# Kernel optimization log

Measured on AMD Instinct MI355X. Metric: run time of the kernel, lower is better.

## Reference

```python
import jax, jax.numpy as jnp
import numpy as np

INPUT_DIM, HIDDEN, OUT_DIM = 7, 64, 4


def _lstm_layer(x_seq, W_ih, W_hh, b_ih, b_hh):
    """Single LSTM layer, batch_first x_seq [B,T,D] -> [B,T,H]. PyTorch gate order i,f,g,o."""
    B = x_seq.shape[0]
    H = W_hh.shape[1]
    # Precompute input projection for all timesteps (hoist GEMM out of the scan).
    x_proj = jnp.einsum('btd,gd->btg', x_seq, W_ih) + b_ih + b_hh  # [B,T,4H]

    def step(carry, xt):
        h, c = carry
        gates = xt + h @ W_hh.T  # [B,4H]
        i, f, g, o = jnp.split(gates, 4, axis=-1)
        i = jax.nn.sigmoid(i)
        f = jax.nn.sigmoid(f)
        g = jnp.tanh(g)
        o = jax.nn.sigmoid(o)
        c = f * c + i * g
        h = o * jnp.tanh(c)
        return (h, c), h

    h0 = jnp.zeros((B, H), x_seq.dtype)
    c0 = jnp.zeros((B, H), x_seq.dtype)
    (_, _), hs = jax.lax.scan(step, (h0, c0), jnp.swapaxes(x_proj, 0, 1))  # hs [T,B,H]
    return jnp.swapaxes(hs, 0, 1)  # [B,T,H]


def setup_inputs() -> dict:
    key = jax.random.key(0)
    ks = jax.random.split(key, 12)
    s = 0.1  # init scale ~ 1/sqrt(hidden)
    x = jax.random.normal(ks[0], (4096, 512, INPUT_DIM), dtype=jnp.float32)
    W_ih0 = jax.random.normal(ks[1], (4 * HIDDEN, INPUT_DIM), dtype=jnp.float32) * s
    W_hh0 = jax.random.normal(ks[2], (4 * HIDDEN, HIDDEN), dtype=jnp.float32) * s
    b_ih0 = jax.random.normal(ks[3], (4 * HIDDEN,), dtype=jnp.float32) * s
    b_hh0 = jax.random.normal(ks[4], (4 * HIDDEN,), dtype=jnp.float32) * s
    W_ih1 = jax.random.normal(ks[5], (4 * HIDDEN, HIDDEN), dtype=jnp.float32) * s
    W_hh1 = jax.random.normal(ks[6], (4 * HIDDEN, HIDDEN), dtype=jnp.float32) * s
    b_ih1 = jax.random.normal(ks[7], (4 * HIDDEN,), dtype=jnp.float32) * s
    b_hh1 = jax.random.normal(ks[8], (4 * HIDDEN,), dtype=jnp.float32) * s
    W_fc = jax.random.normal(ks[9], (OUT_DIM, HIDDEN), dtype=jnp.float32) * s
    b_fc = jax.random.normal(ks[10], (OUT_DIM,), dtype=jnp.float32) * s
    return {"x": x, "W_ih0": W_ih0, "W_hh0": W_hh0, "b_ih0": b_ih0, "b_hh0": b_hh0,
            "W_ih1": W_ih1, "W_hh1": W_hh1, "b_ih1": b_ih1, "b_hh1": b_hh1,
            "W_fc": W_fc, "b_fc": b_fc}


def reference(x, W_ih0, W_hh0, b_ih0, b_hh0, W_ih1, W_hh1, b_ih1, b_hh1, W_fc, b_fc):
    h1 = _lstm_layer(x, W_ih0, W_hh0, b_ih0, b_hh0)   # [B,T,H]
    h2 = _lstm_layer(h1, W_ih1, W_hh1, b_ih1, b_hh1)  # [B,T,H]
    last = h2[:, -1, :]                               # [B,H]
    return last @ W_fc.T + b_fc                       # [B,4]
```

## Files before the change

### kernel.cpp

```cpp
#include <hip/hip_runtime.h>

#define T_SEQ 512
#define HID 64
#define MB 16
#define NTHREADS 1024
#define A1STR 104
#define A2STR 72

typedef __attribute__((ext_vector_type(8))) short short8;
typedef __attribute__((ext_vector_type(4))) float floatx4;

#define LOG2E 1.4426950408889634f

__device__ __forceinline__ short f2bf_rne(float v) {
  unsigned u = __float_as_uint(v);
  return (short)((u + 0x7FFFu + ((u >> 16) & 1u)) >> 16);
}
__device__ __forceinline__ float rcp_(float x) { return __builtin_amdgcn_rcpf(x); }
__device__ __forceinline__ float sigm_p(float ap) {
  return rcp_(1.f + __builtin_amdgcn_exp2f(-ap));
}
__device__ __forceinline__ float tanh_p(float yp) {
  return 1.f - 2.f * rcp_(__builtin_amdgcn_exp2f(yp) + 1.f);
}
__device__ __forceinline__ float tanh_c(float c) {
  return tanh_p((2.f * LOG2E) * c);
}

__device__ __forceinline__ int uofp(int p) {
  return (p & ~7) + ((p & 7) >> 1) + ((p & 1) << 2);
}

__device__ __forceinline__ short w1elem(int k, int n, float wsc,
                                        const float* __restrict__ Wih0,
                                        const float* __restrict__ Whh0) {
  float v;
  if      (k < 64) { v = Whh0[n*64 + uofp(k)]; }
  else if (k < 71) { v = Wih0[n*7 + (k - 64)]; }
  else return (short)0;
  return f2bf_rne(v * wsc);
}
__device__ __forceinline__ short w2elem(int k, int n, float wsc,
                                        const float* __restrict__ Wih1,
                                        const float* __restrict__ Whh1) {
  float v;
  if (k < 64) { v = Wih1[n*64 + uofp(k)]; }
  else        { v = Whh1[n*64 + uofp(k - 64)]; }
  return f2bf_rne(v * wsc);
}

#define MFMA(A, B, C) __builtin_amdgcn_mfma_f32_16x16x32_bf16((A), (B), (C), 0, 0, 0)

#define PACK2(ha, hb)                                                        \
  ((unsigned)(unsigned short)f2bf_rne(ha) |                                  \
   ((unsigned)(unsigned short)f2bf_rne(hb) << 16))

__global__ __launch_bounds__(NTHREADS, 4) void lstm_fused(
    const float* __restrict__ x,
    const float* __restrict__ Wih0, const float* __restrict__ Whh0,
    const float* __restrict__ bih0, const float* __restrict__ bhh0,
    const float* __restrict__ Wih1, const float* __restrict__ Whh1,
    const float* __restrict__ bih1, const float* __restrict__ bhh1,
    const float* __restrict__ Wfc,  const float* __restrict__ bfc,
    float* __restrict__ out)
{
  __shared__ __align__(16) short A1[2][MB][A1STR];
  __shared__ __align__(16) short A2[2][MB][A2STR];
  __shared__ float h2f[MB][HID + 4];

  const int tid  = threadIdx.x;
  const int lane = tid & 63;
  const int wave = tid >> 6;
  const int wl   = wave & 7;
  const bool isL1 = wave < 8;
  const int l15  = lane & 15;
  const int quad = lane >> 4;
  const int quad8= quad * 8;
  const int g4   = l15 & 3;
  const int b0   = blockIdx.x * MB;
  const int u0   = wl*8 + quad;
  const int u1   = u0 + 4;
  const int hpos = wl*8 + 2*quad;
  const int n0   = g4*64 + (wl*8 + (l15 >> 2));
  const int n1   = n0 + 4;
  const float wsc = (g4 == 2) ? 2.f * LOG2E : LOG2E;

  for (int i = tid; i < 2*MB*A1STR/2; i += NTHREADS) ((unsigned*)A1)[i] = 0u;
  for (int i = tid; i < 2*MB*A2STR/2; i += NTHREADS) ((unsigned*)A2)[i] = 0u;

  const float* bi_ = isL1 ? bih0 : bih1;
  const float* bh_ = isL1 ? bhh0 : bhh1;
  floatx4 bia, bib;
  #pragma unroll
  for (int g = 0; g < 4; ++g) {
    float ws = (g == 2) ? 2.f * LOG2E : LOG2E;
    bia[g] = (bi_[g*64 + u0] + bh_[g*64 + u0]) * ws;
    bib[g] = (bi_[g*64 + u1] + bh_[g*64 + u1]) * ws;
  }

  const int xd   = lane & 31;
  const int xrow = 2*wl + (lane >> 5);
  const bool xact = isL1 && (xd < 7);
  const float* xbase = x + ((size_t)(b0 + xrow) * T_SEQ) * 7 + xd;
  float xcur = 0.f;
  if (xact) {
    A1[0][xrow][64 + xd] = f2bf_rne(xbase[0]);
    xcur = xbase[7];
  }

  short8 WA[4], WB[4];
  if (isL1) {
    #pragma unroll
    for (int ks = 0; ks < 3; ++ks) {
      short8 fa, fb;
      #pragma unroll
      for (int jj = 0; jj < 8; ++jj) {
        fa[jj] = w1elem(ks*32 + quad8 + jj, n0, wsc, Wih0, Whh0);
        fb[jj] = w1elem(ks*32 + quad8 + jj, n1, wsc, Wih0, Whh0);
      }
      WA[ks] = fa; WB[ks] = fb;
    }
  } else {
    #pragma unroll
    for (int ks = 0; ks < 4; ++ks) {
      short8 fa, fb;
      #pragma unroll
      for (int jj = 0; jj < 8; ++jj) {
        fa[jj] = w2elem(ks*32 + quad8 + jj, n0, wsc, Wih1, Whh1);
        fb[jj] = w2elem(ks*32 + quad8 + jj, n1, wsc, Wih1, Whh1);
      }
      WA[ks] = fa; WB[ks] = fb;
    }
  }
  __syncthreads();

  float ca = 0.f, cb = 0.f;

#define STEP_X(NXT, XT)                                                      \
    if (xact) {                                                              \
      A1[NXT][xrow][64 + xd] = f2bf_rne(xcur);                               \
      xcur = xbase[7 * (XT)];                                                \
    }

#define EW2(PA, PB, HA, HB)                                                  \
    { float iv = sigm_p(PA[0]), fv = sigm_p(PA[1]);                          \
      float gv = tanh_p(PA[2]), ov = sigm_p(PA[3]);                          \
      ca = fv * ca + iv * gv;  HA = ov * tanh_c(ca); }                       \
    { float iv = sigm_p(PB[0]), fv = sigm_p(PB[1]);                          \
      float gv = tanh_p(PB[2]), ov = sigm_p(PB[3]);                          \
      cb = fv * cb + iv * gv;  HB = ov * tanh_c(cb); }

#define STEP_FULL(CUR, NXT, IT)                                              \
  {                                                                          \
    if (isL1) {                                                              \
      int xt_ = (IT) + 2; if (xt_ > T_SEQ - 1) xt_ = T_SEQ - 1;              \
      STEP_X(NXT, xt_)                                                       \
      short8 hf0 = *(const short8*)&A1[CUR][l15][     quad8];                \
      short8 hf1 = *(const short8*)&A1[CUR][l15][32 + quad8];                \
      short8 hfx = *(const short8*)&A1[CUR][l15][64 + quad8];                \
      floatx4 pa = bia, pb = bib;                                            \
      pa = MFMA(WA[0], hf0, pa);  pb = MFMA(WB[0], hf0, pb);                 \
      pa = MFMA(WA[1], hf1, pa);  pb = MFMA(WB[1], hf1, pb);                 \
      pa = MFMA(WA[2], hfx, pa);  pb = MFMA(WB[2], hfx, pb);                 \
      float ha, hb;                                                          \
      EW2(pa, pb, ha, hb)                                                    \
      *(unsigned*)&A1[NXT][l15][hpos] = PACK2(ha, hb);                       \
    } else {                                                                 \
      short8 hf0 = *(const short8*)&A1[CUR][l15][     quad8];                \
      short8 hf1 = *(const short8*)&A1[CUR][l15][32 + quad8];                \
      short8 h20 = *(const short8*)&A2[CUR][l15][     quad8];                \
      short8 h21 = *(const short8*)&A2[CUR][l15][32 + quad8];                \
      floatx4 pa = bia, pb = bib;                                            \
      pa = MFMA(WA[0], hf0, pa);  pb = MFMA(WB[0], hf0, pb);                 \
      pa = MFMA(WA[1], hf1, pa);  pb = MFMA(WB[1], hf1, pb);                 \
      pa = MFMA(WA[2], h20, pa);  pb = MFMA(WB[2], h20, pb);                 \
      pa = MFMA(WA[3], h21, pa);  pb = MFMA(WB[3], h21, pb);                 \
      float ha, hb;                                                          \
      EW2(pa, pb, ha, hb)                                                    \
      *(unsigned*)&A2[NXT][l15][hpos] = PACK2(ha, hb);                       \
    }                                                                        \
    __syncthreads();                                                         \
  }

  {
    if (isL1) {
      STEP_X(1, 2)
      short8 hf0 = *(const short8*)&A1[0][l15][     quad8];
      short8 hf1 = *(const short8*)&A1[0][l15][32 + quad8];
      short8 hfx = *(const short8*)&A1[0][l15][64 + quad8];
      floatx4 pa = bia, pb = bib;
      pa = MFMA(WA[0], hf0, pa);  pb = MFMA(WB[0], hf0, pb);
      pa = MFMA(WA[1], hf1, pa);  pb = MFMA(WB[1], hf1, pb);
      pa = MFMA(WA[2], hfx, pa);  pb = MFMA(WB[2], hfx, pb);
      float ha, hb;
      EW2(pa, pb, ha, hb)
      *(unsigned*)&A1[1][l15][hpos] = PACK2(ha, hb);
    }
    __syncthreads();
  }

  #pragma unroll 1
  for (int k = 0; k < 255; ++k) {
    STEP_FULL(1, 0, 2*k + 1)
    STEP_FULL(0, 1, 2*k + 2)
  }
  STEP_FULL(1, 0, 511)

  {
    if (!isL1) {
      short8 hf0 = *(const short8*)&A1[0][l15][     quad8];
      short8 hf1 = *(const short8*)&A1[0][l15][32 + quad8];
      short8 h20 = *(const short8*)&A2[0][l15][     quad8];
      short8 h21 = *(const short8*)&A2[0][l15][32 + quad8];
      floatx4 pa = bia, pb = bib;
      pa = MFMA(WA[0], hf0, pa);  pb = MFMA(WB[0], hf0, pb);
      pa = MFMA(WA[1], hf1, pa);  pb = MFMA(WB[1], hf1, pb);
      pa = MFMA(WA[2], h20, pa);  pb = MFMA(WB[2], h20, pb);
      pa = MFMA(WA[3], h21, pa);  pb = MFMA(WB[3], h21, pb);
      float ha, hb;
      EW2(pa, pb, ha, hb)
      h2f[l15][u0] = ha;
      h2f[l15][u1] = hb;
    }
    __syncthreads();
  }

  if (tid < MB * 4) {
    int bbf = tid >> 2, o = tid & 3;
    float acc = bfc[o];
    #pragma unroll 8
    for (int kk = 0; kk < HID; ++kk) acc += h2f[bbf][kk] * Wfc[o*HID + kk];
    out[(size_t)(b0 + bbf) * 4 + o] = acc;
  }
}

extern "C" void kernel_launch(void* const* d_in, const int* in_sizes, int n_in,
                              void* d_out, int out_size, void* d_ws, size_t ws_size,
                              hipStream_t stream) {
  const float* x    = (const float*)d_in[0];
  const float* Wih0 = (const float*)d_in[1];
  const float* Whh0 = (const float*)d_in[2];
  const float* bih0 = (const float*)d_in[3];
  const float* bhh0 = (const float*)d_in[4];
  const float* Wih1 = (const float*)d_in[5];
  const float* Whh1 = (const float*)d_in[6];
  const float* bih1 = (const float*)d_in[7];
  const float* bhh1 = (const float*)d_in[8];
  const float* Wfc  = (const float*)d_in[9];
  const float* bfc  = (const float*)d_in[10];
  (void)d_ws; (void)ws_size; (void)n_in; (void)out_size;

  const int B = in_sizes[0] / (T_SEQ * 7);
  dim3 grid(B / MB);
  lstm_fused<<<grid, NTHREADS, 0, stream>>>(x, Wih0, Whh0, bih0, bhh0,
                                            Wih1, Whh1, bih1, bhh1, Wfc, bfc,
                                            (float*)d_out);
}
```

Before: 447.3 us.

## Rebalance wave roles: 4 layer-2 waves with 4 tiles each, dedicated x-loader waves

Layer 2 now runs on 4 waves that each handle four 16-unit tiles instead of 8 waves handling two tiles each. The remaining 4 waves only stage the next x timestep into LDS, which takes that load off the layer-1 waves. The gate activation math is also rewritten to use fewer reciprocals by folding the sigmoid and tanh divisions together. This cuts contention on the MFMA and transcendental units from layer 2, but makes the layer-2 waves longer per step, so they may become the critical path behind each barrier.

```diff
diff --git a/kernel.cpp b/kernel.cpp
--- a/kernel.cpp
+++ b/kernel.cpp
@@ -5,7 +5,7 @@
 #define MB 16
 #define NTHREADS 1024
 #define A1STR 104
-#define A2STR 72
+#define A2STR 104
 
 typedef __attribute__((ext_vector_type(8))) short short8;
 typedef __attribute__((ext_vector_type(4))) float floatx4;
@@ -17,25 +17,31 @@
   return (short)((u + 0x7FFFu + ((u >> 16) & 1u)) >> 16);
 }
 __device__ __forceinline__ float rcp_(float x) { return __builtin_amdgcn_rcpf(x); }
-__device__ __forceinline__ float sigm_p(float ap) {
-  return rcp_(1.f + __builtin_amdgcn_exp2f(-ap));
-}
-__device__ __forceinline__ float tanh_p(float yp) {
-  return 1.f - 2.f * rcp_(__builtin_amdgcn_exp2f(yp) + 1.f);
-}
-__device__ __forceinline__ float tanh_c(float c) {
-  return tanh_p((2.f * LOG2E) * c);
-}
-
-__device__ __forceinline__ int uofp(int p) {
+__device__ __forceinline__ float exp2_(float x) { return __builtin_amdgcn_exp2f(x); }
+
+__device__ __forceinline__ float gate_h(const floatx4 p, float& c) {
+  float A = exp2_(-p[0]);
+  float F = exp2_(-p[1]);
+  float G = exp2_(p[2]);
+  float O = exp2_(-p[3]);
+  float ig = (G - 1.f) * rcp_((1.f + A) * (G + 1.f));
+  c = rcp_(1.f + F) * c + ig;
+  float C = exp2_((2.f * LOG2E) * c);
+  return (C - 1.f) * rcp_((1.f + O) * (C + 1.f));
+}
+
+__device__ __forceinline__ int U1(int p) {
   return (p & ~7) + ((p & 7) >> 1) + ((p & 1) << 2);
+}
+__device__ __forceinline__ int U2(int p) {
+  return (p & ~15) + ((p & 3) << 2) + ((p >> 2) & 3);
 }
 
 __device__ __forceinline__ short w1elem(int k, int n, float wsc,
                                         const float* __restrict__ Wih0,
                                         const float* __restrict__ Whh0) {
   float v;
-  if      (k < 64) { v = Whh0[n*64 + uofp(k)]; }
+  if      (k < 64) { v = Whh0[n*64 + U1(k)]; }
   else if (k < 71) { v = Wih0[n*7 + (k - 64)]; }
   else return (short)0;
   return f2bf_rne(v * wsc);
@@ -44,8 +50,8 @@
                                         const float* __restrict__ Wih1,
                                         const float* __restrict__ Whh1) {
   float v;
-  if (k < 64) { v = Wih1[n*64 + uofp(k)]; }
-  else        { v = Whh1[n*64 + uofp(k - 64)]; }
+  if (k < 64) { v = Wih1[n*64 + U1(k)]; }
+  else        { v = Whh1[n*64 + U2(k - 64)]; }
   return f2bf_rne(v * wsc);
 }
 
@@ -71,45 +77,41 @@
   const int tid  = threadIdx.x;
   const int lane = tid & 63;
   const int wave = tid >> 6;
-  const int wl   = wave & 7;
-  const bool isL1 = wave < 8;
   const int l15  = lane & 15;
   const int quad = lane >> 4;
   const int quad8= quad * 8;
   const int g4   = l15 & 3;
   const int b0   = blockIdx.x * MB;
+  const bool isL1 = (wave < 8);
+  const bool isL2 = (wave >= 8) && (wave < 12);
+  const float wsc = (g4 == 2) ? 2.f * LOG2E : LOG2E;
+
+  for (int i = tid; i < 2*MB*A1STR/2; i += NTHREADS) ((unsigned*)A1)[i] = 0u;
+  for (int i = tid; i < 2*MB*A2STR/2; i += NTHREADS) ((unsigned*)A2)[i] = 0u;
+
+  const int wl   = wave & 7;
   const int u0   = wl*8 + quad;
   const int u1   = u0 + 4;
   const int hpos = wl*8 + 2*quad;
-  const int n0   = g4*64 + (wl*8 + (l15 >> 2));
-  const int n1   = n0 + 4;
-  const float wsc = (g4 == 2) ? 2.f * LOG2E : LOG2E;
-
-  for (int i = tid; i < 2*MB*A1STR/2; i += NTHREADS) ((unsigned*)A1)[i] = 0u;
-  for (int i = tid; i < 2*MB*A2STR/2; i += NTHREADS) ((unsigned*)A2)[i] = 0u;
-
-  const float* bi_ = isL1 ? bih0 : bih1;
-  const float* bh_ = isL1 ? bhh0 : bhh1;
-  floatx4 bia, bib;
-  #pragma unroll
-  for (int g = 0; g < 4; ++g) {
-    float ws = (g == 2) ? 2.f * LOG2E : LOG2E;
-    bia[g] = (bi_[g*64 + u0] + bh_[g*64 + u0]) * ws;
-    bib[g] = (bi_[g*64 + u1] + bh_[g*64 + u1]) * ws;
-  }
-
-  const int xd   = lane & 31;
-  const int xrow = 2*wl + (lane >> 5);
-  const bool xact = isL1 && (xd < 7);
-  const float* xbase = x + ((size_t)(b0 + xrow) * T_SEQ) * 7 + xd;
+  const int wl2  = wave - 8;
+  const int hbase2 = wl2*16 + quad*4;
+  const int xid  = tid - 768;
+  const bool xact = (wave >= 12) && (xid < MB*7);
+  const int xrow = xid / 7, xd = xid - xrow * 7;
+  const float* xbase = x + ((size_t)(b0 + (xrow & 15)) * T_SEQ) * 7 + xd;
   float xcur = 0.f;
   if (xact) {
     A1[0][xrow][64 + xd] = f2bf_rne(xbase[0]);
     xcur = xbase[7];
   }
 
-  short8 WA[4], WB[4];
+  short8 W1f[3][2];
+  short8 W2f[4][4];
+  floatx4 bA, bB;
+  floatx4 b2[4];
   if (isL1) {
+    const int n0 = g4*64 + (wl*8 + (l15 >> 2));
+    const int n1 = n0 + 4;
     #pragma unroll
     for (int ks = 0; ks < 3; ++ks) {
       short8 fa, fb;
@@ -118,23 +120,38 @@
         fa[jj] = w1elem(ks*32 + quad8 + jj, n0, wsc, Wih0, Whh0);
         fb[jj] = w1elem(ks*32 + quad8 + jj, n1, wsc, Wih0, Whh0);
       }
-      WA[ks] = fa; WB[ks] = fb;
-    }
-  } else {
+      W1f[ks][0] = fa; W1f[ks][1] = fb;
+    }
     #pragma unroll
-    for (int ks = 0; ks < 4; ++ks) {
-      short8 fa, fb;
+    for (int g = 0; g < 4; ++g) {
+      float ws = (g == 2) ? 2.f * LOG2E : LOG2E;
+      bA[g] = (bih0[g*64 + u0] + bhh0[g*64 + u0]) * ws;
+      bB[g] = (bih0[g*64 + u1] + bhh0[g*64 + u1]) * ws;
+    }
+  } else if (isL2) {
+    #pragma unroll
+    for (int t = 0; t < 4; ++t) {
+      const int nt = g4*64 + (wl2*16 + 4*t + (l15 >> 2));
       #pragma unroll
-      for (int jj = 0; jj < 8; ++jj) {
-        fa[jj] = w2elem(ks*32 + quad8 + jj, n0, wsc, Wih1, Whh1);
-        fb[jj] = w2elem(ks*32 + quad8 + jj, n1, wsc, Wih1, Whh1);
+      for (int ks = 0; ks < 4; ++ks) {
+        short8 f;
+        #pragma unroll
+        for (int jj = 0; jj < 8; ++jj)
+          f[jj] = w2elem(ks*32 + quad8 + jj, nt, wsc, Wih1, Whh1);
+        W2f[ks][t] = f;
       }
-      WA[ks] = fa; WB[ks] = fb;
+      const int ut = wl2*16 + 4*t + quad;
+      #pragma unroll
+      for (int g = 0; g < 4; ++g) {
+        float ws = (g == 2) ? 2.f * LOG2E : LOG2E;
+        b2[t][g] = (bih1[g*64 + ut] + bhh1[g*64 + ut]) * ws;
+      }
     }
   }
   __syncthreads();
 
-  float ca = 0.f, cb = 0.f;
+  float c1a = 0.f, c1b = 0.f;
+  float c2s[4] = {0.f, 0.f, 0.f, 0.f};
 
 #define STEP_X(NXT, XT)                                                      \
     if (xact) {                                                              \
@@ -142,60 +159,51 @@
       xcur = xbase[7 * (XT)];                                                \
     }
 
-#define EW2(PA, PB, HA, HB)                                                  \
-    { float iv = sigm_p(PA[0]), fv = sigm_p(PA[1]);                          \
-      float gv = tanh_p(PA[2]), ov = sigm_p(PA[3]);                          \
-      ca = fv * ca + iv * gv;  HA = ov * tanh_c(ca); }                       \
-    { float iv = sigm_p(PB[0]), fv = sigm_p(PB[1]);                          \
-      float gv = tanh_p(PB[2]), ov = sigm_p(PB[3]);                          \
-      cb = fv * cb + iv * gv;  HB = ov * tanh_c(cb); }
-
-#define STEP_FULL(CUR, NXT, IT)                                              \
-  {                                                                          \
-    if (isL1) {                                                              \
-      int xt_ = (IT) + 2; if (xt_ > T_SEQ - 1) xt_ = T_SEQ - 1;              \
-      STEP_X(NXT, xt_)                                                       \
-      short8 hf0 = *(const short8*)&A1[CUR][l15][     quad8];                \
+#define L1_BODY(CUR, NXT)                                                    \
+    { short8 hf0 = *(const short8*)&A1[CUR][l15][     quad8];                \
       short8 hf1 = *(const short8*)&A1[CUR][l15][32 + quad8];                \
       short8 hfx = *(const short8*)&A1[CUR][l15][64 + quad8];                \
-      floatx4 pa = bia, pb = bib;                                            \
-      pa = MFMA(WA[0], hf0, pa);  pb = MFMA(WB[0], hf0, pb);                 \
-      pa = MFMA(WA[1], hf1, pa);  pb = MFMA(WB[1], hf1, pb);                 \
-      pa = MFMA(WA[2], hfx, pa);  pb = MFMA(WB[2], hfx, pb);                 \
-      float ha, hb;                                                          \
-      EW2(pa, pb, ha, hb)                                                    \
-      *(unsigned*)&A1[NXT][l15][hpos] = PACK2(ha, hb);                       \
-    } else {                                                                 \
-      short8 hf0 = *(const short8*)&A1[CUR][l15][     quad8];                \
+      floatx4 pa = bA, pb = bB;                                              \
+      pa = MFMA(W1f[0][0], hf0, pa);  pb = MFMA(W1f[0][1], hf0, pb);         \
+      pa = MFMA(W1f[1][0], hf1, pa);  pb = MFMA(W1f[1][1], hf1, pb);         \
+      pa = MFMA(W1f[2][0], hfx, pa);  pb = MFMA(W1f[2][1], hfx, pb);         \
+      float ha = gate_h(pa, c1a);                                            \
+      float hb = gate_h(pb, c1b);                                            \
+      *(unsigned*)&A1[NXT][l15][hpos] = PACK2(ha, hb); }
+
+#define L2_BODY(CUR, NXT)                                                    \
+    { short8 hf0 = *(const short8*)&A1[CUR][l15][     quad8];                \
       short8 hf1 = *(const short8*)&A1[CUR][l15][32 + quad8];                \
       short8 h20 = *(const short8*)&A2[CUR][l15][     quad8];                \
       short8 h21 = *(const short8*)&A2[CUR][l15][32 + quad8];                \
-      floatx4 pa = bia, pb = bib;                                            \
-      pa = MFMA(WA[0], hf0, pa);  pb = MFMA(WB[0], hf0, pb);                 \
-      pa = MFMA(WA[1], hf1, pa);  pb = MFMA(WB[1], hf1, pb);                 \
-      pa = MFMA(WA[2], h20, pa);  pb = MFMA(WB[2], h20, pb);                 \
-      pa = MFMA(WA[3], h21, pa);  pb = MFMA(WB[3], h21, pb);                 \
-      float ha, hb;                                                          \
-      EW2(pa, pb, ha, hb)                                                    \
-      *(unsigned*)&A2[NXT][l15][hpos] = PACK2(ha, hb);                       \
-    }                                                                        \
+      floatx4 p0 = b2[0], p1 = b2[1], p2v = b2[2], p3 = b2[3];               \
+      p0 = MFMA(W2f[0][0], hf0, p0);  p1 = MFMA(W2f[0][1], hf0, p1);         \
+      p2v= MFMA(W2f[0][2], hf0, p2v); p3 = MFMA(W2f[0][3], hf0, p3);         \
+      p0 = MFMA(W2f[1][0], hf1, p0);  p1 = MFMA(W2f[1][1], hf1, p1);         \
+      p2v= MFMA(W2f[1][2], hf1, p2v); p3 = MFMA(W2f[1][3], hf1, p3);         \
+      p0 = MFMA(W2f[2][0], h20, p0);  p1 = MFMA(W2f[2][1], h20, p1);         \
+      p2v= MFMA(W2f[2][2], h20, p2v); p3 = MFMA(W2f[2][3], h20, p3);         \
+      p0 = MFMA(W2f[3][0], h21, p0);  p1 = MFMA(W2f[3][1], h21, p1);         \
+      p2v= MFMA(W2f[3][2], h21, p2v); p3 = MFMA(W2f[3][3], h21, p3);         \
+      float h0 = gate_h(p0, c2s[0]);                                         \
+      float h1v= gate_h(p1, c2s[1]);                                         \
+      float h2v= gate_h(p2v, c2s[2]);                                        \
+      float h3 = gate_h(p3, c2s[3]);                                         \
+      uint2 pk; pk.x = PACK2(h0, h1v); pk.y = PACK2(h2v, h3);                \
+      *(uint2*)&A2[NXT][l15][hbase2] = pk; }
+
+#define STEP_FULL(CUR, NXT, IT)                                              \
+  {                                                                          \
+    if (isL1) { L1_BODY(CUR, NXT) }                                          \
+    else if (isL2) { L2_BODY(CUR, NXT) }                                     \
+    else { int xt_ = (IT) + 2; if (xt_ > T_SEQ - 1) xt_ = T_SEQ - 1;         \
+           STEP_X(NXT, xt_) }                                                \
     __syncthreads();                                                         \
   }
 
   {
-    if (isL1) {
-      STEP_X(1, 2)
-      short8 hf0 = *(const short8*)&A1[0][l15][     quad8];
-      short8 hf1 = *(const short8*)&A1[0][l15][32 + quad8];
-      short8 hfx = *(const short8*)&A1[0][l15][64 + quad8];
-      floatx4 pa = bia, pb = bib;
-      pa = MFMA(WA[0], hf0, pa);  pb = MFMA(WB[0], hf0, pb);
-      pa = MFMA(WA[1], hf1, pa);  pb = MFMA(WB[1], hf1, pb);
-      pa = MFMA(WA[2], hfx, pa);  pb = MFMA(WB[2], hfx, pb);
-      float ha, hb;
-      EW2(pa, pb, ha, hb)
-      *(unsigned*)&A1[1][l15][hpos] = PACK2(ha, hb);
-    }
+    if (isL1) { L1_BODY(0, 1) }
+    else if (!isL2) { STEP_X(1, 2) }
     __syncthreads();
   }
 
@@ -207,20 +215,24 @@
   STEP_FULL(1, 0, 511)
 
   {
-    if (!isL1) {
+    if (isL2) {
       short8 hf0 = *(const short8*)&A1[0][l15][     quad8];
       short8 hf1 = *(const short8*)&A1[0][l15][32 + quad8];
       short8 h20 = *(const short8*)&A2[0][l15][     quad8];
       short8 h21 = *(const short8*)&A2[0][l15][32 + quad8];
-      floatx4 pa = bia, pb = bib;
-      pa = MFMA(WA[0], hf0, pa);  pb = MFMA(WB[0], hf0, pb);
-      pa = MFMA(WA[1], hf1, pa);  pb = MFMA(WB[1], hf1, pb);
-      pa = MFMA(WA[2], h20, pa);  pb = MFMA(WB[2], h20, pb);
-      pa = MFMA(WA[3], h21, pa);  pb = MFMA(WB[3], h21, pb);
-      float ha, hb;
-      EW2(pa, pb, ha, hb)
-      h2f[l15][u0] = ha;
-      h2f[l15][u1] = hb;
+      floatx4 p0 = b2[0], p1 = b2[1], p2v = b2[2], p3 = b2[3];
+      p0 = MFMA(W2f[0][0], hf0, p0);  p1 = MFMA(W2f[0][1], hf0, p1);
+      p2v= MFMA(W2f[0][2], hf0, p2v); p3 = MFMA(W2f[0][3], hf0, p3);
+      p0 = MFMA(W2f[1][0], hf1, p0);  p1 = MFMA(W2f[1][1], hf1, p1);
+      p2v= MFMA(W2f[1][2], hf1, p2v); p3 = MFMA(W2f[1][3], hf1, p3);
+      p0 = MFMA(W2f[2][0], h20, p0);  p1 = MFMA(W2f[2][1], h20, p1);
+      p2v= MFMA(W2f[2][2], h20, p2v); p3 = MFMA(W2f[2][3], h20, p3);
+      p0 = MFMA(W2f[3][0], h21, p0);  p1 = MFMA(W2f[3][1], h21, p1);
+      p2v= MFMA(W2f[3][2], h21, p2v); p3 = MFMA(W2f[3][3], h21, p3);
+      h2f[l15][wl2*16 +  0 + quad] = gate_h(p0, c2s[0]);
+      h2f[l15][wl2*16 +  4 + quad] = gate_h(p1, c2s[1]);
+      h2f[l15][wl2*16 +  8 + quad] = gate_h(p2v, c2s[2]);
+      h2f[l15][wl2*16 + 12 + quad] = gate_h(p3, c2s[3]);
     }
     __syncthreads();
   }
```

New measurement: 916.1 us. +104.8%, slower.
